# Kernel tuning notes

Hardware: AMD Instinct MI355X
Metric: run time of the kernel (lower is better)

The kernel has to match this reference:

```python
import jax, jax.numpy as jnp
import numpy as np

B, N, K, T = 64, 32768, 128, 512
TMAX = 512  # number of discrete time bins (round(t*10) range)


def setup_inputs() -> dict:
    key = jax.random.key(0)
    k1, k2, k3, k4, k5, k6 = jax.random.split(key, 6)
    state = jax.random.normal(k1, (B, N, 4), dtype=jnp.float32)
    time_idx = jax.random.randint(k2, (B, N), 0, TMAX, dtype=jnp.int32)
    # unique_ids in [-1, K-1]; -1 marks clutter (invalid) measurements
    unique_ids = jax.random.randint(k3, (B, N), 0, K + 1, dtype=jnp.int32) - 1
    # trajectory states [B,K,T,5]: cols [x, y, vx, vy, t] with round(t*10) in 0..TMAX-1
    xy = jax.random.normal(k4, (B, K, T, 2), dtype=jnp.float32)
    vel = jax.random.normal(k5, (B, K, T, 2), dtype=jnp.float32)
    # per-(b,k) permutation of 0..T-1 -> unique times within each trajectory
    times = jnp.argsort(jax.random.uniform(k6, (B, K, T)), axis=-1).astype(jnp.float32)
    traj_states = jnp.concatenate([xy, vel, (times / 10.0)[..., None]], axis=-1)
    return {"state": state, "time_idx": time_idx, "unique_ids": unique_ids,
            "traj_states": traj_states}


def reference(state, time_idx, unique_ids, traj_states):
    xy = state[..., :2]                                   # [B,N,2]
    tvals = jnp.round(traj_states[..., 4] * 10.0).astype(jnp.int32)  # [B,K,T]
    traj_xy = traj_states[..., :2]                        # [B,K,T,2]
    # dense lookup table [B,K,TMAX,2]; default 0 matches torch.zeros_like(tgt)
    b_ix = jnp.arange(B)[:, None, None]
    k_ix = jnp.arange(K)[None, :, None]
    table = jnp.zeros((B, K, TMAX, 2), dtype=state.dtype)
    table = table.at[b_ix, k_ix, tvals].set(traj_xy, mode="drop")
    # gather tgt per measurement by (object id, time bin)
    obj = jnp.clip(unique_ids, 0, K - 1)
    tcl = jnp.clip(time_idx, 0, TMAX - 1)
    tgt = table[jnp.arange(B)[:, None], obj, tcl]         # [B,N,2]
    valid = unique_ids >= 0
    tgt = jnp.where(valid[..., None], tgt, 0.0)
    diff = jnp.abs(xy - tgt).sum(-1)                      # [B,N]
    vf = valid.astype(state.dtype)
    loss = (diff * vf).sum() / vf.sum()
    return loss
```

## Files before the change

kernel.cpp:

```cpp
#include <hip/hip_runtime.h>
#include <hip/hip_fp16.h>

constexpr int Bc = 64;
constexpr int Nc = 32768;
constexpr int Kc = 128;
constexpr int Tc = 512;
constexpr int TMAXc = 512;
constexpr int BK = Bc * Kc;

typedef float f32x4 __attribute__((ext_vector_type(4)));
typedef float f32x2 __attribute__((ext_vector_type(2)));
typedef int   i32x2 __attribute__((ext_vector_type(2)));

constexpr size_t TABLE_BYTES = (size_t)BK * TMAXc * 4;
constexpr int NBLK1 = BK / 2;
constexpr int NBLK2 = 512;

__global__ __launch_bounds__(256) void build_table_k(
    const f32x4* __restrict__ traj4,
    uint2* __restrict__ table2)
{
    __shared__ __align__(16) float    stage[2 * Tc * 5];
    __shared__ __align__(8)  unsigned tbl[2 * TMAXc];

    const int j   = blockIdx.x;
    const int xcd = j & 7;
    const int s   = j >> 3;
    const int b   = ((s >> 6) << 3) | xcd;
    const int k2  = s & 63;
    const int bk0 = (b << 7) | (k2 << 1);

    const f32x4* src = traj4 + (size_t)bk0 * 640;
    #pragma unroll
    for (int r = 0; r < 5; ++r) {
        int t = threadIdx.x + r * 256;
        ((f32x4*)stage)[t] = __builtin_nontemporal_load(&src[t]);
    }
    __syncthreads();

    #pragma unroll
    for (int r = 0; r < 4; ++r) {
        int t = threadIdx.x + r * 256;
        float x  = stage[t * 5 + 0];
        float y  = stage[t * 5 + 1];
        float tv = stage[t * 5 + 4];
        int tau = __float2int_rn(tv * 10.0f);
        if ((unsigned)tau < (unsigned)TMAXc) {
            __half2 p = __floats2half2_rn(x, y);
            unsigned raw;
            __builtin_memcpy(&raw, &p, 4);
            tbl[((t >> 9) << 9) + tau] = raw;
        }
    }
    __syncthreads();

    uint2* dst = table2 + (size_t)bk0 * 256;
    #pragma unroll
    for (int r = 0; r < 2; ++r) {
        int t = threadIdx.x + r * 256;
        dst[t] = ((const uint2*)tbl)[t];
    }
}

__global__ __launch_bounds__(256) void gather_reduce_k(
    const f32x4*    __restrict__ state4,
    const i32x2*    __restrict__ tidx2,
    const i32x2*    __restrict__ uid2,
    const unsigned* __restrict__ table,
    float2*         __restrict__ partials)
{
    const int j     = blockIdx.x;
    const int xcd   = j & 7;
    const int s     = j >> 3;
    const int b     = ((s >> 3) << 3) | xcd;
    const int chunk = s & 7;
    const int bpair = (b << 14) + (chunk << 11);
    const unsigned* tb = table + ((long long)b << 16);

    f32x4    sv[8];
    i32x2    idv[8], tiv[8];
    unsigned tg[16];

    #pragma unroll
    for (int r = 0; r < 8; ++r) {
        int p = bpair + r * 256 + threadIdx.x;
        sv[r]  = __builtin_nontemporal_load(&state4[p]);
        idv[r] = __builtin_nontemporal_load(&uid2[p]);
        tiv[r] = __builtin_nontemporal_load(&tidx2[p]);
    }
    f32x2 sw[8];
    #pragma unroll
    for (int r = 0; r < 8; ++r) {
        int p = bpair + r * 256 + threadIdx.x;
        sw[r] = __builtin_nontemporal_load(
            (const f32x2*)&state4[2 * (size_t)p + 1]);
    }
    #pragma unroll
    for (int r = 0; r < 8; ++r) {
        int p = bpair + r * 256 + threadIdx.x;
        sv[r] = __builtin_nontemporal_load(&state4[2 * (size_t)p]);
    }

    #pragma unroll
    for (int r = 0; r < 8; ++r) {
        int o0 = min(max(idv[r].x, 0), Kc - 1);
        int t0 = min(max(tiv[r].x, 0), TMAXc - 1);
        int o1 = min(max(idv[r].y, 0), Kc - 1);
        int t1 = min(max(tiv[r].y, 0), TMAXc - 1);
        tg[2 * r]     = tb[(o0 << 9) + t0];
        tg[2 * r + 1] = tb[(o1 << 9) + t1];
    }

    float sum = 0.0f, cnt = 0.0f;
    #pragma unroll
    for (int r = 0; r < 8; ++r) {
        __half2 p0, p1;
        __builtin_memcpy(&p0, &tg[2 * r], 4);
        __builtin_memcpy(&p1, &tg[2 * r + 1], 4);
        if (idv[r].x >= 0) {
            sum += fabsf(sv[r].x - __low2float(p0)) + fabsf(sv[r].y - __high2float(p0));
            cnt += 1.0f;
        }
        if (idv[r].y >= 0) {
            sum += fabsf(sw[r].x - __low2float(p1)) + fabsf(sw[r].y - __high2float(p1));
            cnt += 1.0f;
        }
    }

    #pragma unroll
    for (int off = 32; off > 0; off >>= 1) {
        sum += __shfl_down(sum, off, 64);
        cnt += __shfl_down(cnt, off, 64);
    }
    __shared__ float2 lred[4];
    const int lane = threadIdx.x & 63;
    const int w    = threadIdx.x >> 6;
    if (lane == 0) lred[w] = make_float2(sum, cnt);
    __syncthreads();
    if (threadIdx.x == 0) {
        float s2 = 0.0f, c2 = 0.0f;
        #pragma unroll
        for (int q = 0; q < 4; ++q) { s2 += lred[q].x; c2 += lred[q].y; }
        partials[j] = make_float2(s2, c2);
    }
}

__global__ __launch_bounds__(512) void final_reduce_k(
    const float2* __restrict__ partials, float* __restrict__ out)
{
    float s, c;
    {
        float2 p = partials[threadIdx.x];
        s = p.x; c = p.y;
    }
    #pragma unroll
    for (int off = 32; off > 0; off >>= 1) {
        s += __shfl_down(s, off, 64);
        c += __shfl_down(c, off, 64);
    }
    __shared__ float2 lds[8];
    int lane = threadIdx.x & 63;
    int w    = threadIdx.x >> 6;
    if (lane == 0) lds[w] = make_float2(s, c);
    __syncthreads();
    if (threadIdx.x == 0) {
        float s2 = 0.0f, c2 = 0.0f;
        #pragma unroll
        for (int q = 0; q < 8; ++q) { s2 += lds[q].x; c2 += lds[q].y; }
        out[0] = s2 / c2;
    }
}

extern "C" void kernel_launch(void* const* d_in, const int* in_sizes, int n_in,
                              void* d_out, int out_size, void* d_ws, size_t ws_size,
                              hipStream_t stream) {
    const f32x4* state4 = (const f32x4*)d_in[0];
    const i32x2* tidx2  = (const i32x2*)d_in[1];
    const i32x2* uid2   = (const i32x2*)d_in[2];
    const f32x4* traj4  = (const f32x4*)d_in[3];
    float* out = (float*)d_out;

    unsigned* table    = (unsigned*)d_ws;
    float2*   partials = (float2*)((char*)d_ws + TABLE_BYTES);

    build_table_k  <<<NBLK1, 256, 0, stream>>>(traj4, (uint2*)table);
    gather_reduce_k<<<NBLK2, 256, 0, stream>>>(state4, tidx2, uid2, table, partials);
    final_reduce_k <<<1, 512, 0, stream>>>(partials, out);
}
```

Baseline: 39.62 us.

## Stage per-object table slice in LDS and scan all measurements per block

Each gather block loads a 16-object slice of the batch's lookup table into shared memory. It then scans every measurement in the batch, accumulating only those whose object id maps to its slice. This replaces scattered global table reads with LDS reads. The cost is that each block reads ids, time indices and state for the whole batch, multiplying input traffic by eight.

```diff
diff --git a/kernel.cpp b/kernel.cpp
--- a/kernel.cpp
+++ b/kernel.cpp
@@ -63,67 +63,75 @@
 }
 
 __global__ __launch_bounds__(256) void gather_reduce_k(
-    const f32x4*    __restrict__ state4,
+    const f32x2*    __restrict__ state2,
     const i32x2*    __restrict__ tidx2,
     const i32x2*    __restrict__ uid2,
-    const unsigned* __restrict__ table,
+    const uint2*    __restrict__ table2,
     float2*         __restrict__ partials)
 {
-    const int j     = blockIdx.x;
-    const int xcd   = j & 7;
-    const int s     = j >> 3;
-    const int b     = ((s >> 3) << 3) | xcd;
-    const int chunk = s & 7;
-    const int bpair = (b << 14) + (chunk << 11);
-    const unsigned* tb = table + ((long long)b << 16);
+    __shared__ unsigned tbl[16 * TMAXc];
+    __shared__ float2 lred[4];
 
-    f32x4    sv[8];
-    i32x2    idv[8], tiv[8];
-    unsigned tg[16];
+    const int j   = blockIdx.x;
+    const int xcd = j & 7;
+    const int s   = j >> 3;
+    const int b   = ((s >> 3) << 3) | xcd;
+    const int q   = s & 7;
 
+    const uint2* slice = table2 + ((size_t)b << 15) + (q << 12);
     #pragma unroll
-    for (int r = 0; r < 8; ++r) {
-        int p = bpair + r * 256 + threadIdx.x;
-        sv[r]  = __builtin_nontemporal_load(&state4[p]);
-        idv[r] = __builtin_nontemporal_load(&uid2[p]);
-        tiv[r] = __builtin_nontemporal_load(&tidx2[p]);
+    for (int r = 0; r < 16; ++r) {
+        int t = threadIdx.x + r * 256;
+        ((uint2*)tbl)[t] = slice[t];
     }
-    f32x2 sw[8];
-    #pragma unroll
-    for (int r = 0; r < 8; ++r) {
-        int p = bpair + r * 256 + threadIdx.x;
-        sw[r] = __builtin_nontemporal_load(
-            (const f32x2*)&state4[2 * (size_t)p + 1]);
-    }
-    #pragma unroll
-    for (int r = 0; r < 8; ++r) {
-        int p = bpair + r * 256 + threadIdx.x;
-        sv[r] = __builtin_nontemporal_load(&state4[2 * (size_t)p]);
-    }
+    __syncthreads();
 
-    #pragma unroll
-    for (int r = 0; r < 8; ++r) {
-        int o0 = min(max(idv[r].x, 0), Kc - 1);
-        int t0 = min(max(tiv[r].x, 0), TMAXc - 1);
-        int o1 = min(max(idv[r].y, 0), Kc - 1);
-        int t1 = min(max(tiv[r].y, 0), TMAXc - 1);
-        tg[2 * r]     = tb[(o0 << 9) + t0];
-        tg[2 * r + 1] = tb[(o1 << 9) + t1];
-    }
+    const int pbase = b << 14;
+    float sum = 0.0f, cnt = 0.0f;
 
-    float sum = 0.0f, cnt = 0.0f;
-    #pragma unroll
-    for (int r = 0; r < 8; ++r) {
-        __half2 p0, p1;
-        __builtin_memcpy(&p0, &tg[2 * r], 4);
-        __builtin_memcpy(&p1, &tg[2 * r + 1], 4);
-        if (idv[r].x >= 0) {
-            sum += fabsf(sv[r].x - __low2float(p0)) + fabsf(sv[r].y - __high2float(p0));
-            cnt += 1.0f;
+    #pragma unroll 1
+    for (int c = 0; c < 8; ++c) {
+        i32x2 u[8], tv[8];
+        #pragma unroll
+        for (int r = 0; r < 8; ++r) {
+            int p = pbase + (c << 11) + (r << 8) + threadIdx.x;
+            u[r]  = uid2[p];
+            tv[r] = tidx2[p];
         }
-        if (idv[r].y >= 0) {
-            sum += fabsf(sw[r].x - __low2float(p1)) + fabsf(sw[r].y - __high2float(p1));
-            cnt += 1.0f;
+        unsigned g[16];
+        #pragma unroll
+        for (int r = 0; r < 8; ++r) {
+            int o0 = min(max(u[r].x, 0), Kc - 1);
+            int o1 = min(max(u[r].y, 0), Kc - 1);
+            int t0 = min(max(tv[r].x, 0), TMAXc - 1);
+            int t1 = min(max(tv[r].y, 0), TMAXc - 1);
+            g[2*r]   = tbl[((o0 & 15) << 9) | t0];
+            g[2*r+1] = tbl[((o1 & 15) << 9) | t1];
+        }
+        f32x2 s0[8], s1[8];
+        #pragma unroll
+        for (int r = 0; r < 8; ++r) {
+            int p = pbase + (c << 11) + (r << 8) + threadIdx.x;
+            s0[r] = state2[4 * (size_t)p];
+            s1[r] = state2[4 * (size_t)p + 2];
+        }
+        #pragma unroll
+        for (int r = 0; r < 8; ++r) {
+            int o0 = min(max(u[r].x, 0), Kc - 1);
+            int o1 = min(max(u[r].y, 0), Kc - 1);
+            __half2 p0, p1;
+            __builtin_memcpy(&p0, &g[2*r], 4);
+            __builtin_memcpy(&p1, &g[2*r+1], 4);
+            if (u[r].x >= 0 && (o0 >> 4) == q) {
+                sum += fabsf(s0[r].x - __low2float(p0)) +
+                       fabsf(s0[r].y - __high2float(p0));
+                cnt += 1.0f;
+            }
+            if (u[r].y >= 0 && (o1 >> 4) == q) {
+                sum += fabsf(s1[r].x - __low2float(p1)) +
+                       fabsf(s1[r].y - __high2float(p1));
+                cnt += 1.0f;
+            }
         }
     }
 
@@ -132,7 +140,6 @@
         sum += __shfl_down(sum, off, 64);
         cnt += __shfl_down(cnt, off, 64);
     }
-    __shared__ float2 lred[4];
     const int lane = threadIdx.x & 63;
     const int w    = threadIdx.x >> 6;
     if (lane == 0) lred[w] = make_float2(sum, cnt);
@@ -140,7 +147,7 @@
     if (threadIdx.x == 0) {
         float s2 = 0.0f, c2 = 0.0f;
         #pragma unroll
-        for (int q = 0; q < 4; ++q) { s2 += lred[q].x; c2 += lred[q].y; }
+        for (int t = 0; t < 4; ++t) { s2 += lred[t].x; c2 += lred[t].y; }
         partials[j] = make_float2(s2, c2);
     }
 }
@@ -166,7 +173,7 @@
     if (threadIdx.x == 0) {
         float s2 = 0.0f, c2 = 0.0f;
         #pragma unroll
-        for (int q = 0; q < 8; ++q) { s2 += lds[q].x; c2 += lds[q].y; }
+        for (int t = 0; t < 8; ++t) { s2 += lds[t].x; c2 += lds[t].y; }
         out[0] = s2 / c2;
     }
 }
@@ -174,7 +181,7 @@
 extern "C" void kernel_launch(void* const* d_in, const int* in_sizes, int n_in,
                               void* d_out, int out_size, void* d_ws, size_t ws_size,
                               hipStream_t stream) {
-    const f32x4* state4 = (const f32x4*)d_in[0];
+    const f32x2* state2 = (const f32x2*)d_in[0];
     const i32x2* tidx2  = (const i32x2*)d_in[1];
     const i32x2* uid2   = (const i32x2*)d_in[2];
     const f32x4* traj4  = (const f32x4*)d_in[3];
@@ -184,6 +191,7 @@
     float2*   partials = (float2*)((char*)d_ws + TABLE_BYTES);
 
     build_table_k  <<<NBLK1, 256, 0, stream>>>(traj4, (uint2*)table);
-    gather_reduce_k<<<NBLK2, 256, 0, stream>>>(state4, tidx2, uid2, table, partials);
+    gather_reduce_k<<<NBLK2, 256, 0, stream>>>(state2, tidx2, uid2,
+                                               (const uint2*)table, partials);
     final_reduce_k <<<1, 512, 0, stream>>>(partials, out);
 }
```

New measurement: 46.86 us. 1.18x slower.
